# Kernel tuning notes

Measured on AMD Instinct MI355X. Metric: run time of the kernel, lower is better.

## Reference

```python
import jax, jax.numpy as jnp
import numpy as np

B, T, C, H = 8, 2048, 256, 4
D = C // H  # head_dim = 64
SCALE = D ** -0.5


def setup_inputs() -> dict:
    key = jax.random.key(0)
    ks = jax.random.split(key, 5)
    return {
        "x": jax.random.normal(ks[0], (B, T, C), dtype=jnp.float32),
        "Wqkv": jax.random.normal(ks[1], (C, 3 * C), dtype=jnp.float32) * (C ** -0.5),
        "bqkv": jax.random.normal(ks[2], (3 * C,), dtype=jnp.float32) * 0.02,
        "Wproj": jax.random.normal(ks[3], (C, C), dtype=jnp.float32) * (C ** -0.5),
        "bproj": jax.random.normal(ks[4], (C,), dtype=jnp.float32) * 0.02,
    }


def reference(x, Wqkv, bqkv, Wproj, bproj):
    b, t, c = x.shape
    # QKV projection -> (3, B, H, T, D) matching torch permute(2,0,3,1,4)
    qkv = (x @ Wqkv + bqkv).reshape(b, t, 3, H, D)
    qkv = jnp.transpose(qkv, (2, 0, 3, 1, 4))
    q, k, v = qkv[0], qkv[1], qkv[2]  # each (B, H, T, D)
    # Full T x T scores (faithful to the original non-fused implementation)
    attn = jnp.einsum("bhqd,bhkd->bhqk", q, k) * SCALE
    causal = jnp.triu(jnp.ones((t, t), dtype=bool), k=1)  # True above diagonal
    attn = jnp.where(causal, -jnp.inf, attn)
    attn = jax.nn.softmax(attn, axis=-1)
    # dropout is identity in eval mode
    out = jnp.einsum("bhqk,bhkd->bhqd", attn, v)  # (B, H, T, D)
    out = jnp.transpose(out, (0, 2, 1, 3)).reshape(b, t, c)
    return out @ Wproj + bproj
```

## Files before the change

### kernel.cpp

```cpp
#include <hip/hip_runtime.h>
#include <hip/hip_bf16.h>
#include <math.h>

#define BATCH 8
#define SEQ   2048
#define CH    256
#define NH    4
#define HD    64
#define NQB   (SEQ / 64)
#define QSCALE 0.18033688011112042f

typedef short  bfrag __attribute__((ext_vector_type(8)));
typedef float  ffrag __attribute__((ext_vector_type(4)));
typedef unsigned short ushort_t;
typedef unsigned int u32;

__device__ __forceinline__ unsigned short f2bf(float f) {
    union { float f; unsigned int u; } v; v.f = f;
    unsigned int r = v.u + 0x7FFF + ((v.u >> 16) & 1);
    return (unsigned short)(r >> 16);
}
__device__ __forceinline__ unsigned int pack2(float a, float b) {
    const __hip_bfloat162 p = __float22bfloat162_rn(make_float2(a, b));
    return *(const unsigned int*)&p;
}
__device__ __forceinline__ void gload16(const ushort_t* g, ushort_t* l) {
    __builtin_amdgcn_global_load_lds(
        (const __attribute__((address_space(1))) u32*)g,
        (__attribute__((address_space(3))) u32*)l, 16, 0, 0);
}

#define WQN (CH * 3 * CH)
#define WPN (CH * CH)
#define XN  (BATCH * SEQ * CH)
#define XN8 (XN / 8)

__global__ __launch_bounds__(256) void prep_kernel(
    const float* __restrict__ x,
    const float* __restrict__ Wqkv, const float* __restrict__ Wproj,
    ushort_t* __restrict__ xb,
    ushort_t* __restrict__ WqkvT, ushort_t* __restrict__ WprojT) {
    const int fid = blockIdx.x * 256 + threadIdx.x;
    if (fid < XN8) {
        const float4 a = *(const float4*)&x[(size_t)fid * 8];
        const float4 c = *(const float4*)&x[(size_t)fid * 8 + 4];
        uint4 pk;
        pk.x = pack2(a.x, a.y); pk.y = pack2(a.z, a.w);
        pk.z = pack2(c.x, c.y); pk.w = pack2(c.z, c.w);
        *(uint4*)&xb[(size_t)fid * 8] = pk;
    } else {
        const int id = fid - XN8;
        if (id < WQN) {
            const int n = id >> 8, k = id & 255;
            WqkvT[n * CH + k] = f2bf(Wqkv[k * (3 * CH) + n]);
        } else if (id < WQN + WPN) {
            const int i = id - WQN;
            const int n = i >> 8, k = i & 255;
            WprojT[n * CH + k] = f2bf(Wproj[k * CH + n]);
        }
    }
}

#define GLS 72

__global__ __launch_bounds__(256) void qkv_mfma_kernel(
    const ushort_t* __restrict__ xb, const ushort_t* __restrict__ Wt,
    const float* __restrict__ bias,
    ushort_t* __restrict__ Qb, ushort_t* __restrict__ Kb,
    ushort_t* __restrict__ Vtb) {
    __shared__ ushort_t smem[128 * 136];
    ushort_t* As = smem;
    ushort_t* Bs = smem + 128 * 64;

    const int tid = threadIdx.x;
    const int wv  = tid >> 6;
    const int ln  = tid & 63;
    const int l15 = ln & 15;
    const int l4  = ln >> 4;
    const int e   = l15 & 7;
    const int wr  = wv >> 1;
    const int wc  = wv & 1;
    const int n0  = blockIdx.x * 128;
    const int m0  = blockIdx.y * 128;

    const int grow = ln >> 3;
    const int swz  = ((ln & 7) ^ grow) * 8;

    ffrag acc[4][4];
    #pragma unroll
    for (int i = 0; i < 4; i++)
        #pragma unroll
        for (int j = 0; j < 4; j++) acc[i][j] = (ffrag){0.f, 0.f, 0.f, 0.f};

    for (int k0 = 0; k0 < CH; k0 += 64) {
        #pragma unroll
        for (int i = 0; i < 4; i++) {
            const int rowA = (i * 4 + wv) * 8 + grow;
            gload16(&xb[(size_t)(m0 + rowA) * CH + k0 + swz], &As[(i * 4 + wv) * 512]);
            gload16(&Wt[(size_t)(n0 + rowA) * CH + k0 + swz], &Bs[(i * 4 + wv) * 512]);
        }
        __syncthreads();
        #pragma unroll
        for (int kk = 0; kk < 64; kk += 32) {
            bfrag a[4], b[4];
            #pragma unroll
            for (int i = 0; i < 4; i++) {
                const int R = wr * 64 + i * 16 + l15;
                a[i] = *(const bfrag*)&As[R * 64 + ((((kk >> 3) + l4) ^ e) * 8)];
            }
            #pragma unroll
            for (int j = 0; j < 4; j++) {
                const int R = wc * 64 + j * 16 + l15;
                b[j] = *(const bfrag*)&Bs[R * 64 + ((((kk >> 3) + l4) ^ e) * 8)];
            }
            #pragma unroll
            for (int i = 0; i < 4; i++)
                #pragma unroll
                for (int j = 0; j < 4; j++)
                    acc[i][j] = __builtin_amdgcn_mfma_f32_16x16x32_bf16(a[i], b[j], acc[i][j], 0, 0, 0);
        }
        __syncthreads();
    }

    const int mat = n0 >> 8;
    const int b   = m0 >> 11;
    const int t0  = m0 & (SEQ - 1);
    ushort_t (*T)[136] = (ushort_t(*)[136])smem;

    if (mat < 2) {
        const float sc = (mat == 0) ? QSCALE : 1.0f;
        #pragma unroll
        for (int j = 0; j < 4; j++) {
            const int n_local = wc * 64 + j * 16 + l15;
            const float bj = bias[n0 + n_local];
            #pragma unroll
            for (int i = 0; i < 4; i++) {
                const int m_base = wr * 64 + i * 16 + l4 * 4;
                #pragma unroll
                for (int r = 0; r < 4; r++)
                    T[m_base + r][n_local] = f2bf((acc[i][j][r] + bj) * sc);
            }
        }
        __syncthreads();
        ushort_t* dst = (mat == 0) ? Qb : Kb;
        #pragma unroll
        for (int rr = 0; rr < 8; rr++) {
            const int fid = tid + rr * 256;
            const int row = fid >> 4;
            const int c8  = (fid & 15) * 8;
            const int n_glob = n0 + c8;
            const int h = (n_glob >> 6) & 3;
            const int d = n_glob & 63;
            *(uint4*)&dst[((size_t)((b * NH + h) * SEQ) + t0 + row) * HD + d] =
                *(const uint4*)&T[row][c8];
        }
    } else {
        #pragma unroll
        for (int j = 0; j < 4; j++) {
            const int n_local = wc * 64 + j * 16 + l15;
            const float bj = bias[n0 + n_local];
            #pragma unroll
            for (int i = 0; i < 4; i++) {
                const int m_base = wr * 64 + i * 16 + l4 * 4;
                ushort4 pk;
                pk.x = f2bf(acc[i][j][0] + bj);
                pk.y = f2bf(acc[i][j][1] + bj);
                pk.z = f2bf(acc[i][j][2] + bj);
                pk.w = f2bf(acc[i][j][3] + bj);
                *(ushort4*)&T[n_local][m_base] = pk;
            }
        }
        __syncthreads();
        #pragma unroll
        for (int rr = 0; rr < 8; rr++) {
            const int fid = tid + rr * 256;
            const int row = fid >> 4;
            const int c8  = (fid & 15) * 8;
            const int n_glob = n0 + row;
            const int h = (n_glob >> 6) & 3;
            const int d = n_glob & 63;
            *(uint4*)&Vtb[(size_t)((b * NH + h) * HD + d) * SEQ + t0 + c8] =
                *(const uint4*)&T[row][c8];
        }
    }
}

__global__ __launch_bounds__(256, 4) void attn_mfma_kernel(
    const ushort_t* __restrict__ Qb, const ushort_t* __restrict__ Kb,
    const ushort_t* __restrict__ Vtb, ushort_t* __restrict__ out) {
    __shared__ ushort_t Ps[64 * 64];
    __shared__ ushort_t KV[4 * 64 * 64];

    const int tid = threadIdx.x;
    const int wv  = tid >> 6;
    const int ln  = tid & 63;
    const int l15 = ln & 15;
    const int l4  = ln >> 4;
    const int e   = l15 & 7;

    const int L  = blockIdx.x;
    const int g  = L & 255;
    const int s4 = L >> 8;
    const int v  = g >> 5;
    const int qb = (s4 == 0) ? (31 - v) : (s4 == 1) ? (16 + v) : (s4 == 2) ? (15 - v) : v;
    const int bh = g & 31;
    const int b  = bh >> 2;
    const int h  = bh & 3;

    const ushort_t* Qp = Qb + ((size_t)(bh * SEQ + qb * 64 + wv * 16 + l15)) * HD + l4 * 8;
    const bfrag bq0 = *(const bfrag*)Qp;
    const bfrag bq1 = *(const bfrag*)(Qp + 32);

    const ushort_t* Kbase = Kb  + (size_t)bh * SEQ * HD;
    const ushort_t* Vbase = Vtb + (size_t)bh * HD * SEQ;
    const int srow  = tid >> 3;
    const int sc    = tid & 7;
    const int goffA = srow * 64 + sc * 8;
    const int voffA = srow * SEQ + sc * 8;
    const int soffA = srow * 64 + ((sc ^ (srow & 7)) * 8);

    const int kf0 = l15 * 64 + ((l4 ^ e) * 8);
    const int pf0 = (wv * 16 + l15) * 64 + ((l4 ^ e) * 8);
    const int pp  = e >> 1;
    const int pwb = (wv * 16 + l15) * 64 + (((l4 >> 1) ^ (e & 1)) * 8) + (l4 & 1) * 4;

    uint4 kK0, kK1, kV0, kV1;
    kK0 = *(const uint4*)&Kbase[goffA];
    kK1 = *(const uint4*)&Kbase[goffA + 32 * 64];
    kV0 = *(const uint4*)&Vbase[voffA];
    kV1 = *(const uint4*)&Vbase[voffA + 32 * SEQ];
    *(uint4*)&KV[soffA]          = kK0;
    *(uint4*)&KV[soffA + 2048]   = kK1;
    *(uint4*)&KV[8192 + soffA]        = kV0;
    *(uint4*)&KV[8192 + soffA + 2048] = kV1;
    if (qb >= 1) {
        kK0 = *(const uint4*)&Kbase[4096 + goffA];
        kK1 = *(const uint4*)&Kbase[4096 + goffA + 32 * 64];
        kV0 = *(const uint4*)&Vbase[64 + voffA];
        kV1 = *(const uint4*)&Vbase[64 + voffA + 32 * SEQ];
    }

    ffrag o[4];
    #pragma unroll
    for (int n = 0; n < 4; n++) o[n] = (ffrag){0.f, 0.f, 0.f, 0.f};
    float l_q = 0.f;
    const int qg_l = qb * 64 + wv * 16 + l15;

    for (int kt = 0; kt <= qb; kt++) {
        if (kt > 0) {
            const int kb = (kt & 1) * 4096;
            *(uint4*)&KV[kb + soffA]          = kK0;
            *(uint4*)&KV[kb + soffA + 2048]   = kK1;
            *(uint4*)&KV[8192 + kb + soffA]        = kV0;
            *(uint4*)&KV[8192 + kb + soffA + 2048] = kV1;
            if (kt < qb) {
                const ushort_t* Kp  = Kbase + (kt + 1) * 4096;
                const ushort_t* Vtp = Vbase + (kt + 1) * 64;
                kK0 = *(const uint4*)&Kp[goffA];
                kK1 = *(const uint4*)&Kp[goffA + 32 * 64];
                kV0 = *(const uint4*)&Vtp[voffA];
                kV1 = *(const uint4*)&Vtp[voffA + 32 * SEQ];
            }
        }
        __syncthreads();

        const ushort_t* Kbuf = KV + (kt & 1) * 4096;
        const ushort_t* Vbuf = KV + 8192 + (kt & 1) * 4096;

        ffrag s[4];
        __builtin_amdgcn_s_setprio(1);
        #pragma unroll
        for (int n = 0; n < 4; n++) {
            const bfrag ak0 = *(const bfrag*)&Kbuf[n * 1024 + kf0];
            const bfrag ak1 = *(const bfrag*)&Kbuf[n * 1024 + (kf0 ^ 32)];
            ffrag z = (ffrag){0.f, 0.f, 0.f, 0.f};
            z = __builtin_amdgcn_mfma_f32_16x16x32_bf16(ak0, bq0, z, 0, 0, 0);
            z = __builtin_amdgcn_mfma_f32_16x16x32_bf16(ak1, bq1, z, 0, 0, 0);
            s[n] = z;
        }
        __builtin_amdgcn_s_setprio(0);
        if (kt == qb) {
            #pragma unroll
            for (int n = 0; n < 4; n++)
                #pragma unroll
                for (int r = 0; r < 4; r++)
                    if (kt * 64 + n * 16 + l4 * 4 + r > qg_l) s[n][r] = -INFINITY;
        }

        #pragma unroll
        for (int n = 0; n < 4; n++)
            #pragma unroll
            for (int r = 0; r < 4; r++) {
                const float p = __builtin_amdgcn_exp2f(s[n][r]);
                s[n][r] = p;
                l_q += p;
            }

        #pragma unroll
        for (int n = 0; n < 4; n++) {
            uint2 pk;
            pk.x = pack2(s[n][0], s[n][1]);
            pk.y = pack2(s[n][2], s[n][3]);
            *(uint2*)&Ps[pwb + ((n ^ pp) << 4)] = pk;
        }

        const bfrag ap0 = *(const bfrag*)&Ps[pf0];
        const bfrag ap1 = *(const bfrag*)&Ps[pf0 ^ 32];
        __builtin_amdgcn_s_setprio(1);
        #pragma unroll
        for (int n = 0; n < 4; n++) {
            const bfrag av0 = *(const bfrag*)&Vbuf[n * 1024 + kf0];
            const bfrag av1 = *(const bfrag*)&Vbuf[n * 1024 + (kf0 ^ 32)];
            o[n] = __builtin_amdgcn_mfma_f32_16x16x32_bf16(av0, ap0, o[n], 0, 0, 0);
            o[n] = __builtin_amdgcn_mfma_f32_16x16x32_bf16(av1, ap1, o[n], 0, 0, 0);
        }
        __builtin_amdgcn_s_setprio(0);
    }

    l_q += __shfl_xor(l_q, 16);
    l_q += __shfl_xor(l_q, 32);

    const float li = 1.0f / l_q;
    const int tq = qb * 64 + wv * 16 + l15;
    ushort_t* op = out + (size_t)(b * SEQ + tq) * CH + h * HD;
    #pragma unroll
    for (int n = 0; n < 4; n++) {
        ushort4 pk;
        pk.x = f2bf(o[n][0] * li);
        pk.y = f2bf(o[n][1] * li);
        pk.z = f2bf(o[n][2] * li);
        pk.w = f2bf(o[n][3] * li);
        *(ushort4*)&op[n * 16 + l4 * 4] = pk;
    }
}

__global__ __launch_bounds__(256) void proj_mfma_kernel(
    const ushort_t* __restrict__ Ab, const ushort_t* __restrict__ Wt,
    const float* __restrict__ bias, float* __restrict__ O) {
    __shared__ ushort_t smem[(128 + 64) * GLS];
    ushort_t* As = smem;
    ushort_t* Bs = smem + 128 * GLS;

    const int tid = threadIdx.x;
    const int wv  = tid >> 6;
    const int ln  = tid & 63;
    const int l15 = ln & 15;
    const int l4  = ln >> 4;
    const int wr  = wv >> 1;
    const int wc  = wv & 1;
    const int n0  = blockIdx.x * 64;
    const int m0  = blockIdx.y * 128;

    ffrag acc[4][2];
    #pragma unroll
    for (int i = 0; i < 4; i++)
        #pragma unroll
        for (int j = 0; j < 2; j++) acc[i][j] = (ffrag){0.f, 0.f, 0.f, 0.f};

    for (int k0 = 0; k0 < CH; k0 += 64) {
        #pragma unroll
        for (int r = 0; r < 4; r++) {
            const int fid = tid + r * 256;
            const int row = fid >> 3, c8 = (fid & 7) * 8;
            *(uint4*)&As[row * GLS + c8] = *(const uint4*)&Ab[(size_t)(m0 + row) * CH + k0 + c8];
        }
        #pragma unroll
        for (int r = 0; r < 2; r++) {
            const int fid = tid + r * 256;
            const int row = fid >> 3, c8 = (fid & 7) * 8;
            *(uint4*)&Bs[row * GLS + c8] = *(const uint4*)&Wt[(n0 + row) * CH + k0 + c8];
        }
        __syncthreads();
        #pragma unroll
        for (int kk = 0; kk < 64; kk += 32) {
            bfrag a[4], b[2];
            #pragma unroll
            for (int i = 0; i < 4; i++)
                a[i] = *(const bfrag*)&As[(wr * 64 + i * 16 + l15) * GLS + kk + l4 * 8];
            #pragma unroll
            for (int j = 0; j < 2; j++)
                b[j] = *(const bfrag*)&Bs[(wc * 32 + j * 16 + l15) * GLS + kk + l4 * 8];
            #pragma unroll
            for (int i = 0; i < 4; i++)
                #pragma unroll
                for (int j = 0; j < 2; j++)
                    acc[i][j] = __builtin_amdgcn_mfma_f32_16x16x32_bf16(a[i], b[j], acc[i][j], 0, 0, 0);
        }
        __syncthreads();
    }

    #pragma unroll
    for (int j = 0; j < 2; j++) {
        const int n = n0 + wc * 32 + j * 16 + l15;
        const float bj = bias[n];
        #pragma unroll
        for (int i = 0; i < 4; i++) {
            const int m = m0 + wr * 64 + i * 16 + l4 * 4;
            #pragma unroll
            for (int r = 0; r < 4; r++)
                O[(size_t)(m + r) * CH + n] = acc[i][j][r] + bj;
        }
    }
}

extern "C" void kernel_launch(void* const* d_in, const int* in_sizes, int n_in,
                              void* d_out, int out_size, void* d_ws, size_t ws_size,
                              hipStream_t stream) {
    const float* x     = (const float*)d_in[0];
    const float* Wqkv  = (const float*)d_in[1];
    const float* bqkv  = (const float*)d_in[2];
    const float* Wproj = (const float*)d_in[3];
    const float* bproj = (const float*)d_in[4];
    float* out = (float*)d_out;

    const size_t BHTD = (size_t)BATCH * NH * SEQ * HD;
    ushort_t* WqkvT  = (ushort_t*)d_ws;
    ushort_t* WprojT = WqkvT + (size_t)3 * CH * CH;
    ushort_t* Qb     = WprojT + (size_t)CH * CH;
    ushort_t* Kb     = Qb + BHTD;
    ushort_t* Vtb    = Kb + BHTD;
    ushort_t* attn_b = Vtb + BHTD;
    ushort_t* xb     = attn_b;

    const int M = BATCH * SEQ;

    {
        const int total = XN8 + WQN + WPN;
        prep_kernel<<<(total + 255) / 256, 256, 0, stream>>>(x, Wqkv, Wproj, xb, WqkvT, WprojT);
    }
    {
        dim3 grid((3 * CH) / 128, M / 128);
        qkv_mfma_kernel<<<grid, 256, 0, stream>>>(xb, WqkvT, bqkv, Qb, Kb, Vtb);
    }
    {
        attn_mfma_kernel<<<dim3(NQB * BATCH * NH), 256, 0, stream>>>(Qb, Kb, Vtb, attn_b);
    }
    {
        dim3 grid(CH / 64, M / 128);
        proj_mfma_kernel<<<grid, 256, 0, stream>>>(attn_b, WprojT, bproj, out);
    }
}
```

Before: 133.5 us.

## Use direct global-to-LDS loads in attention and stage proj epilogue through LDS

The attention kernel stops staging K/V tiles through registers and instead issues direct global-to-LDS loads (gload16) into a double buffer, with the XOR swizzle moved onto the global address side and one sync per iteration. This is meant to cut register pressure and the VGPR round trip so the next tile can prefetch while MFMAs run. The projection kernel now writes its accumulators into a padded LDS tile and then stores coalesced float4 rows instead of scattered scalar stores. This adds an extra barrier and LDS traffic in the epilogue. The gload16 helper is assumed to be defined in the unseen part of the file.

After: 137.5 us. 1.03x slower.

```diff
diff --git a/kernel.cpp b/kernel.cpp
--- a/kernel.cpp
+++ b/kernel.cpp
@@ -213,32 +213,21 @@
 
     const ushort_t* Kbase = Kb  + (size_t)bh * SEQ * HD;
     const ushort_t* Vbase = Vtb + (size_t)bh * HD * SEQ;
-    const int srow  = tid >> 3;
-    const int sc    = tid & 7;
-    const int goffA = srow * 64 + sc * 8;
-    const int voffA = srow * SEQ + sc * 8;
-    const int soffA = srow * 64 + ((sc ^ (srow & 7)) * 8);
+    const int srow   = tid >> 3;
+    const int schunk = ((tid & 7) ^ (srow & 7)) * 8;
+    const int goffK  = srow * 64 + schunk;
+    const int goffV  = srow * SEQ + schunk;
+    ushort_t* const dstW = &KV[wv * 512];
 
     const int kf0 = l15 * 64 + ((l4 ^ e) * 8);
     const int pf0 = (wv * 16 + l15) * 64 + ((l4 ^ e) * 8);
     const int pp  = e >> 1;
     const int pwb = (wv * 16 + l15) * 64 + (((l4 >> 1) ^ (e & 1)) * 8) + (l4 & 1) * 4;
 
-    uint4 kK0, kK1, kV0, kV1;
-    kK0 = *(const uint4*)&Kbase[goffA];
-    kK1 = *(const uint4*)&Kbase[goffA + 32 * 64];
-    kV0 = *(const uint4*)&Vbase[voffA];
-    kV1 = *(const uint4*)&Vbase[voffA + 32 * SEQ];
-    *(uint4*)&KV[soffA]          = kK0;
-    *(uint4*)&KV[soffA + 2048]   = kK1;
-    *(uint4*)&KV[8192 + soffA]        = kV0;
-    *(uint4*)&KV[8192 + soffA + 2048] = kV1;
-    if (qb >= 1) {
-        kK0 = *(const uint4*)&Kbase[4096 + goffA];
-        kK1 = *(const uint4*)&Kbase[4096 + goffA + 32 * 64];
-        kV0 = *(const uint4*)&Vbase[64 + voffA];
-        kV1 = *(const uint4*)&Vbase[64 + voffA + 32 * SEQ];
-    }
+    gload16(Kbase + goffK,            dstW);
+    gload16(Kbase + goffK + 2048,     dstW + 2048);
+    gload16(Vbase + goffV,            dstW + 8192);
+    gload16(Vbase + goffV + 32 * SEQ, dstW + 8192 + 2048);
 
     ffrag o[4];
     #pragma unroll
@@ -247,22 +236,17 @@
     const int qg_l = qb * 64 + wv * 16 + l15;
 
     for (int kt = 0; kt <= qb; kt++) {
-        if (kt > 0) {
-            const int kb = (kt & 1) * 4096;
-            *(uint4*)&KV[kb + soffA]          = kK0;
-            *(uint4*)&KV[kb + soffA + 2048]   = kK1;
-            *(uint4*)&KV[8192 + kb + soffA]        = kV0;
-            *(uint4*)&KV[8192 + kb + soffA + 2048] = kV1;
-            if (kt < qb) {
-                const ushort_t* Kp  = Kbase + (kt + 1) * 4096;
-                const ushort_t* Vtp = Vbase + (kt + 1) * 64;
-                kK0 = *(const uint4*)&Kp[goffA];
-                kK1 = *(const uint4*)&Kp[goffA + 32 * 64];
-                kV0 = *(const uint4*)&Vtp[voffA];
-                kV1 = *(const uint4*)&Vtp[voffA + 32 * SEQ];
-            }
-        }
-        __syncthreads();
+        __syncthreads();
+
+        if (kt < qb) {
+            const int kb = ((kt + 1) & 1) * 4096;
+            const ushort_t* Kp = Kbase + (kt + 1) * 4096;
+            const ushort_t* Vp = Vbase + (kt + 1) * 64;
+            gload16(Kp + goffK,            dstW + kb);
+            gload16(Kp + goffK + 2048,     dstW + kb + 2048);
+            gload16(Vp + goffV,            dstW + 8192 + kb);
+            gload16(Vp + goffV + 32 * SEQ, dstW + 8192 + kb + 2048);
+        }
 
         const ushort_t* Kbuf = KV + (kt & 1) * 4096;
         const ushort_t* Vbuf = KV + 8192 + (kt & 1) * 4096;
@@ -337,9 +321,9 @@
 __global__ __launch_bounds__(256) void proj_mfma_kernel(
     const ushort_t* __restrict__ Ab, const ushort_t* __restrict__ Wt,
     const float* __restrict__ bias, float* __restrict__ O) {
-    __shared__ ushort_t smem[(128 + 64) * GLS];
-    ushort_t* As = smem;
-    ushort_t* Bs = smem + 128 * GLS;
+    __shared__ __align__(16) char smem_raw[128 * 68 * 4];
+    ushort_t* As = (ushort_t*)smem_raw;
+    ushort_t* Bs = As + 128 * GLS;
 
     const int tid = threadIdx.x;
     const int wv  = tid >> 6;
@@ -389,17 +373,27 @@
         __syncthreads();
     }
 
+    float (*Tf)[68] = (float(*)[68])smem_raw;
     #pragma unroll
     for (int j = 0; j < 2; j++) {
-        const int n = n0 + wc * 32 + j * 16 + l15;
-        const float bj = bias[n];
+        const int n_local = wc * 32 + j * 16 + l15;
+        const float bj = bias[n0 + n_local];
         #pragma unroll
         for (int i = 0; i < 4; i++) {
-            const int m = m0 + wr * 64 + i * 16 + l4 * 4;
+            const int m_base = wr * 64 + i * 16 + l4 * 4;
             #pragma unroll
             for (int r = 0; r < 4; r++)
-                O[(size_t)(m + r) * CH + n] = acc[i][j][r] + bj;
-        }
+                Tf[m_base + r][n_local] = acc[i][j][r] + bj;
+        }
+    }
+    __syncthreads();
+    #pragma unroll
+    for (int rr = 0; rr < 8; rr++) {
+        const int fid = tid + rr * 256;
+        const int row = fid >> 4;
+        const int c4  = (fid & 15) * 4;
+        *(float4*)&O[(size_t)(m0 + row) * CH + n0 + c4] =
+            *(const float4*)&Tf[row][c4];
     }
 }
 
```
